# Performance work log

Measured on AMD Instinct MI355X. Metric: run time of the kernel, lower is better.

Reference implementation:

```python
import jax, jax.numpy as jnp
import numpy as np

B, N, D, H, S = 64, 1000, 512, 8, 20
DK = D // H
TANH_CLIP = 10.0
NEG = -1e9


def setup_inputs() -> dict:
    key = jax.random.key(0)
    k1, k2, k3, k4, k5 = jax.random.split(key, 5)
    embeddings = jax.random.normal(k1, (B, N, D), dtype=jnp.float32)
    q = jax.random.normal(k2, (B, S, D), dtype=jnp.float32)
    # action_mask: True = feasible. Ensure at least one feasible node per row.
    action_mask = jax.random.bernoulli(k3, 0.5, (B, S, N))
    action_mask = action_mask.at[:, :, 0].set(True)
    W_kvl = jax.random.normal(k4, (D, 3 * D), dtype=jnp.float32) * (1.0 / np.sqrt(D))
    W_out = jax.random.normal(k5, (D, D), dtype=jnp.float32) * (1.0 / np.sqrt(D))
    return {"embeddings": embeddings, "q": q, "action_mask": action_mask,
            "W_kvl": W_kvl, "W_out": W_out}


def reference(embeddings, q, action_mask, W_kvl, W_out):
    # _precompute: project node embeddings into glimpse K, V and logit K
    kvl = jnp.einsum('bnd,de->bne', embeddings, W_kvl)  # [B,N,3D]
    glimpse_k, glimpse_v, logit_k = jnp.split(kvl, 3, axis=-1)
    # dynamic embedding is zero (StaticEmbedding for TSP)

    mask = ~action_mask  # True = infeasible, shape [B,S,N]

    # multi-head glimpse attention
    qh = q.reshape(B, S, H, DK)
    kh = glimpse_k.reshape(B, N, H, DK)
    vh = glimpse_v.reshape(B, N, H, DK)
    compat = jnp.einsum('bshd,bnhd->bhsn', qh, kh) / np.sqrt(DK)
    compat = jnp.where(mask[:, None, :, :], NEG, compat)
    attn = jax.nn.softmax(compat, axis=-1)
    heads = jnp.einsum('bhsn,bnhd->bshd', attn, vh).reshape(B, S, D)
    glimpse = jnp.einsum('bsd,de->bse', heads, W_out)  # [B,S,D]

    # pointer logits against logit_k, tanh clipping, mask, log-softmax
    logits = jnp.einsum('bsd,bnd->bsn', glimpse, logit_k) / np.sqrt(D)
    logits = TANH_CLIP * jnp.tanh(logits)
    logits = jnp.where(mask, NEG, logits)
    log_p = jax.nn.log_softmax(logits, axis=-1)  # [B,S,N]

    # rearrange 'b s l -> (s b) l'
    return jnp.swapaxes(log_p, 0, 1).reshape(S * B, N)
```

## Files before the change

### kernel.cpp

```cpp
#include <hip/hip_runtime.h>

#define BB 64
#define NN 1000
#define NP 1024
#define DD 512
#define HH 8
#define SS 20
#define NEGV -1e9f

typedef float v4f __attribute__((ext_vector_type(4)));
typedef short v8s __attribute__((ext_vector_type(8)));
typedef int   v8i __attribute__((ext_vector_type(8)));
typedef int   v4i __attribute__((ext_vector_type(4)));
typedef unsigned char uchar;
typedef unsigned long long ulong_t;

static __device__ __forceinline__ short f2bf(float f) {
    unsigned u = __builtin_bit_cast(unsigned, f);
    u = (u + 0x7fffu + ((u >> 16) & 1u)) >> 16;
    return (short)u;
}
static __device__ __forceinline__ float bf2f(short s) {
    unsigned u = ((unsigned)(unsigned short)s) << 16;
    return __builtin_bit_cast(float, u);
}
static __device__ __forceinline__ uchar f2fp8(float f) {
    return (uchar)(__builtin_amdgcn_cvt_pk_fp8_f32(f, 0.f, 0, false) & 0xff);
}

static __device__ __forceinline__ void gld16(const void* g, void* l) {
    __builtin_amdgcn_global_load_lds(
        (const __attribute__((address_space(1))) void*)(g),
        (__attribute__((address_space(3))) void*)(l),
        16, 0, 0);
}

__global__ void prep(const float* __restrict__ Wkvl, uchar* __restrict__ Wt8,
                     const float* __restrict__ Wout, short* __restrict__ Wot,
                     const float* __restrict__ emb, int* __restrict__ emb8) {
    __shared__ float t[32][33];
    int bid = blockIdx.x, tid = threadIdx.x;
    if (bid < 768) {
        int c0 = (bid % 48) * 32, r0 = (bid / 48) * 32;
        int x = tid & 31, y = tid >> 5;
        for (int k = 0; k < 32; k += 8)
            t[y + k][x] = Wkvl[(long)(r0 + y + k) * 1536 + c0 + x];
        __syncthreads();
        for (int k = 0; k < 32; k += 8)
            Wt8[(long)(c0 + y + k) * 512 + r0 + x] = f2fp8(t[x][y + k]);
    } else if (bid < 1024) {
        int bb = bid - 768;
        int c0 = (bb & 15) * 32, r0 = (bb >> 4) * 32;
        int x = tid & 31, y = tid >> 5;
        for (int k = 0; k < 32; k += 8)
            t[y + k][x] = Wout[(long)(r0 + y + k) * 512 + c0 + x];
        __syncthreads();
        for (int k = 0; k < 32; k += 8)
            Wot[(long)(c0 + y + k) * 512 + r0 + x] = f2bf(t[x][y + k]);
    } else {
        int i = (bid - 1024) * 256 + tid;
        long o = (long)i * 8;
        v4f a = *(const v4f*)(emb + o);
        v4f b = *(const v4f*)(emb + o + 4);
        int lo = __builtin_amdgcn_cvt_pk_fp8_f32(a.x, a.y, 0, false);
        lo = __builtin_amdgcn_cvt_pk_fp8_f32(a.z, a.w, lo, true);
        int hi = __builtin_amdgcn_cvt_pk_fp8_f32(b.x, b.y, 0, false);
        hi = __builtin_amdgcn_cvt_pk_fp8_f32(b.z, b.w, hi, true);
        int2 r; r.x = lo; r.y = hi;
        *(int2*)(emb8 + i * 2) = r;
    }
}

__global__ __launch_bounds__(256) void gemm_kvl(const uchar* __restrict__ emb8,
                                                const uchar* __restrict__ Wt8,
                                                uchar* __restrict__ kvl8) {
    extern __shared__ __align__(16) uchar smem[];
    uchar* As0 = smem;
    uchar* Bs0 = smem + 32768;
    int tid = threadIdx.x;
    int id = blockIdx.x;
    int wgid = (id & 7) * 750 + (id >> 3);
    int m_idx = wgid / 12, n_idx = wgid - m_idx * 12;
    int m0 = m_idx * 128, n0 = n_idx * 128;
    int wid = tid >> 6, lane = tid & 63, quad = lane >> 4, l16 = lane & 15;
    int wm = wid & 1, wn = wid >> 1;
    const uchar* Ag = emb8 + (long)m0 * 512;
    const uchar* Bg = Wt8 + (long)n0 * 512;
    int rsub = lane >> 3;
    int kc = ((lane & 7) ^ rsub) * 16;

    v4f acc[4][4] = {};

    auto stageAB = [&](int bi, int kk) {
        #pragma unroll
        for (int p = 0; p < 4; ++p) {
            int rl = wid * 32 + p * 8;
            gld16(Ag + (long)(rl + rsub) * 512 + kk + kc, As0 + bi * 16384 + rl * 128);
        }
        #pragma unroll
        for (int p = 0; p < 4; ++p) {
            int rl = wid * 32 + p * 8;
            gld16(Bg + (long)(rl + rsub) * 512 + kk + kc, Bs0 + bi * 16384 + rl * 128);
        }
    };
    auto ldfrag = [&](const uchar* base, int row) -> v8i {
        int c0 = (quad * 2) ^ (row & 7);
        v4i lo = *(const v4i*)(base + row * 128 + c0 * 16);
        v4i hi = *(const v4i*)(base + row * 128 + (c0 ^ 1) * 16);
        return __builtin_shufflevector(lo, hi, 0, 1, 2, 3, 4, 5, 6, 7);
    };

    stageAB(0, 0);
    stageAB(1, 128);
    asm volatile("s_waitcnt vmcnt(8)" ::: "memory");
    __builtin_amdgcn_s_barrier();
    __builtin_amdgcn_sched_barrier(0);

    v8i af[4], bf[4];
    #pragma unroll
    for (int t = 0; t < 4; ++t) {
        int cur = t & 1;
        const uchar* ab = As0 + cur * 16384;
        const uchar* bb = Bs0 + cur * 16384;
        #pragma unroll
        for (int i = 0; i < 4; ++i) af[i] = ldfrag(ab, wm * 64 + i * 16 + l16);
        #pragma unroll
        for (int j = 0; j < 4; ++j) bf[j] = ldfrag(bb, wn * 64 + j * 16 + l16);
        __builtin_amdgcn_s_setprio(1);
        #pragma unroll
        for (int i = 0; i < 4; ++i)
            #pragma unroll
            for (int j = 0; j < 2; ++j)
                acc[i][j] = __builtin_amdgcn_mfma_scale_f32_16x16x128_f8f6f4(
                    af[i], bf[j], acc[i][j], 0, 0, 0, 0x7f7f7f7f, 0, 0x7f7f7f7f);
        __builtin_amdgcn_s_setprio(0);
        asm volatile("s_waitcnt lgkmcnt(0)" ::: "memory");
        __builtin_amdgcn_s_barrier();
        if (t < 2) stageAB(cur, (t + 2) * 128);
        __builtin_amdgcn_s_setprio(1);
        #pragma unroll
        for (int i = 0; i < 4; ++i)
            #pragma unroll
            for (int j = 2; j < 4; ++j)
                acc[i][j] = __builtin_amdgcn_mfma_scale_f32_16x16x128_f8f6f4(
                    af[i], bf[j], acc[i][j], 0, 0, 0, 0x7f7f7f7f, 0, 0x7f7f7f7f);
        __builtin_amdgcn_s_setprio(0);
        if (t < 3) {
            if (t < 2) asm volatile("s_waitcnt vmcnt(8)" ::: "memory");
            else       asm volatile("s_waitcnt vmcnt(0)" ::: "memory");
            __builtin_amdgcn_s_barrier();
            __builtin_amdgcn_sched_barrier(0);
        }
    }
    __syncthreads();

    short* rp = (short*)smem;
    short* r = rp + wid * (16 * 72);
    #pragma unroll
    for (int i = 0; i < 4; ++i) {
        #pragma unroll
        for (int jj = 0; jj < 4; ++jj)
            #pragma unroll
            for (int rr = 0; rr < 4; ++rr)
                r[(quad * 4 + rr) * 72 + jj * 16 + l16] = f2bf(acc[i][jj][rr]);
        #pragma unroll
        for (int h = 0; h < 2; ++h) {
            int rowl = h * 8 + (lane >> 3);
            int colc = (lane & 7) * 8;
            v8s val = *(const v8s*)(r + rowl * 72 + colc);
            int lo = __builtin_amdgcn_cvt_pk_fp8_f32(bf2f(val[0]), bf2f(val[1]), 0, false);
            lo = __builtin_amdgcn_cvt_pk_fp8_f32(bf2f(val[2]), bf2f(val[3]), lo, true);
            int hi = __builtin_amdgcn_cvt_pk_fp8_f32(bf2f(val[4]), bf2f(val[5]), 0, false);
            hi = __builtin_amdgcn_cvt_pk_fp8_f32(bf2f(val[6]), bf2f(val[7]), hi, true);
            int2 st; st.x = lo; st.y = hi;
            *(int2*)(kvl8 + (long)(m0 + wm * 64 + i * 16 + rowl) * 1536 +
                     n0 + wn * 64 + colc) = st;
        }
    }
}

__global__ void transpose_v(const uchar* __restrict__ kvl8, uchar* __restrict__ Vt8) {
    int bh = blockIdx.x, b = bh >> 3, h = bh & 7;
    int n0 = blockIdx.y * 64;
    __shared__ uchar T[64][72];
    int tid = threadIdx.x;
    #pragma unroll
    for (int it = 0; it < 2; ++it) {
        int nl = (tid >> 3) + it * 32;
        int n = n0 + nl;
        int nc = n < NN ? n : NN - 1;
        int d0 = (tid & 7) * 8;
        ulong_t v = *(const ulong_t*)(kvl8 + ((long)b * NN + nc) * 1536 + DD + h * 64 + d0);
        uchar* vb = (uchar*)&v;
        #pragma unroll
        for (int j = 0; j < 8; ++j) T[d0 + j][nl] = vb[j];
    }
    __syncthreads();
    #pragma unroll
    for (int it = 0; it < 2; ++it) {
        int d = (tid >> 3) + it * 32;
        int ns = (tid & 7) * 8;
        *(ulong_t*)(Vt8 + ((long)bh * 64 + d) * NP + n0 + ns) = *(const ulong_t*)&T[d][ns];
    }
}

#define CST 1036
__global__ __launch_bounds__(512) void attn_fused(const float* __restrict__ q,
                                                  const uchar* __restrict__ kvl8,
                                                  const uchar* __restrict__ Vt8,
                                                  const int* __restrict__ mask,
                                                  float* __restrict__ heads) {
    int b = blockIdx.x, h = blockIdx.y;
    __shared__ __align__(16) uchar qs[32 * 72];
    __shared__ __align__(16) short cmp[SS * CST];
    int tid = threadIdx.x, wid = tid >> 6, lane = tid & 63, quad = lane >> 4, l16 = lane & 15;
    for (int i = tid; i < 32 * 64; i += 512) {
        int row = i >> 6, col = i & 63;
        float v = (row < SS) ? q[((long)b * SS + row) * DD + h * 64 + col] : 0.f;
        qs[row * 72 + col] = f2fp8(v);
    }
    __syncthreads();
    long af[2][2];
    #pragma unroll
    for (int mt = 0; mt < 2; ++mt)
        #pragma unroll
        for (int ks = 0; ks < 2; ++ks)
            af[mt][ks] = *(const long*)(qs + (mt * 16 + l16) * 72 + ks * 32 + quad * 8);
    for (int t = 0; t < 8; ++t) {
        int nt = wid * 8 + t;
        int n = nt * 16 + l16;
        int nc = n < NN ? n : NN - 1;
        const uchar* kp = kvl8 + ((long)b * NN + nc) * 1536 + h * 64 + quad * 8;
        long b0 = *(const long*)kp;
        long b1 = *(const long*)(kp + 32);
        #pragma unroll
        for (int mt = 0; mt < 2; ++mt) {
            v4f a = {};
            a = __builtin_amdgcn_mfma_f32_16x16x32_fp8_fp8(af[mt][0], b0, a, 0, 0, 0);
            a = __builtin_amdgcn_mfma_f32_16x16x32_fp8_fp8(af[mt][1], b1, a, 0, 0, 0);
            #pragma unroll
            for (int r = 0; r < 4; ++r) {
                int s = mt * 16 + quad * 4 + r;
                if (s < SS) cmp[s * CST + nt * 16 + l16] = f2bf(a[r] * 0.125f);
            }
        }
    }
    __syncthreads();
    for (int s = wid; s < SS; s += 8) {
        const int* mr = mask + ((long)b * SS + s) * NN;
        float x[16];
        float mx = NEGV;
        #pragma unroll
        for (int i = 0; i < 16; ++i) {
            int n = lane + 64 * i;
            float v = bf2f(cmp[s * CST + n]);
            bool feas = (n < NN) && (mr[n < NN ? n : 0] != 0);
            x[i] = feas ? v : NEGV;
            mx = fmaxf(mx, x[i]);
        }
        for (int off = 32; off; off >>= 1) mx = fmaxf(mx, __shfl_xor(mx, off));
        float sum = 0.f;
        #pragma unroll
        for (int i = 0; i < 16; ++i) { x[i] = __expf(x[i] - mx); sum += x[i]; }
        for (int off = 32; off; off >>= 1) sum += __shfl_xor(sum, off);
        float inv = 1.0f / sum;
        uchar* pr = (uchar*)cmp + (long)s * (CST * 2);
        #pragma unroll
        for (int i = 0; i < 16; ++i) pr[lane + 64 * i] = f2fp8(x[i] * inv);
    }
    __syncthreads();
    int mt = wid & 1, dt = wid >> 1;
    int srow = mt * 16 + l16; if (srow > SS - 1) srow = SS - 1;
    const uchar* ap = (const uchar*)cmp + (long)srow * (CST * 2) + quad * 8;
    const uchar* vb = Vt8 + (long)(b * HH + h) * 64 * NP;
    v4f acc = {};
    for (int k0 = 0; k0 < NP; k0 += 32) {
        long afr = *(const long*)(ap + k0);
        long bfr = *(const long*)(vb + (long)(dt * 16 + l16) * NP + k0 + quad * 8);
        acc = __builtin_amdgcn_mfma_f32_16x16x32_fp8_fp8(afr, bfr, acc, 0, 0, 0);
    }
    #pragma unroll
    for (int r = 0; r < 4; ++r) {
        int s = mt * 16 + quad * 4 + r;
        if (s < SS)
            heads[((long)b * SS + s) * DD + h * 64 + dt * 16 + l16] = acc[r];
    }
}

__global__ __launch_bounds__(256) void out_proj(const float* __restrict__ heads,
                                                const short* __restrict__ Wot,
                                                float* __restrict__ glimpse) {
    __shared__ __align__(16) short As[64 * 40], Bs[64 * 40];
    int tid = threadIdx.x;
    int m0 = blockIdx.x * 64, n0 = blockIdx.y * 64;
    int wid = tid >> 6, lane = tid & 63, quad = lane >> 4, l16 = lane & 15;
    int wm = wid & 1, wn = wid >> 1;
    int arow = tid >> 3, akol = (tid & 7) * 4;
    int brow = tid >> 2, bkol = (tid & 3) * 8;
    v4f acc[2][2] = {};
    for (int kk = 0; kk < 512; kk += 32) {
        #pragma unroll
        for (int p = 0; p < 2; ++p) {
            int r = arow + p * 32;
            v4f a = *(const v4f*)(heads + (long)(m0 + r) * 512 + kk + akol);
            short4 s4;
            s4.x = f2bf(a.x); s4.y = f2bf(a.y); s4.z = f2bf(a.z); s4.w = f2bf(a.w);
            *(short4*)(As + r * 40 + akol) = s4;
        }
        *(uint4*)(Bs + brow * 40 + bkol) =
            *(const uint4*)(Wot + (long)(n0 + brow) * 512 + kk + bkol);
        __syncthreads();
        #pragma unroll
        for (int i = 0; i < 2; ++i) {
            v8s af = *(const v8s*)(As + (wm * 32 + i * 16 + l16) * 40 + quad * 8);
            #pragma unroll
            for (int j = 0; j < 2; ++j) {
                v8s bf = *(const v8s*)(Bs + (wn * 32 + j * 16 + l16) * 40 + quad * 8);
                acc[i][j] = __builtin_amdgcn_mfma_f32_16x16x32_bf16(af, bf, acc[i][j], 0, 0, 0);
            }
        }
        __syncthreads();
    }
    #pragma unroll
    for (int i = 0; i < 2; ++i)
        #pragma unroll
        for (int j = 0; j < 2; ++j)
            #pragma unroll
            for (int r = 0; r < 4; ++r)
                glimpse[(long)(m0 + wm * 32 + i * 16 + quad * 4 + r) * 512 +
                        n0 + wn * 32 + j * 16 + l16] = acc[i][j][r];
}

__global__ __launch_bounds__(256) void ptr_logits(const float* __restrict__ glimpse,
                                                  const uchar* __restrict__ kvl8,
                                                  float* __restrict__ logits) {
    int b = blockIdx.x, g = blockIdx.y;
    __shared__ __align__(16) uchar Gs[32 * 520];
    int tid = threadIdx.x;
    #pragma unroll
    for (int it = 0; it < 16; ++it) {
        int e = it * 1024 + tid * 4;
        int row = e >> 9, col = e & 511;
        int pk = 0;
        if (row < SS) {
            v4f a = *(const v4f*)(glimpse + ((long)b * SS + row) * 512 + col);
            pk = __builtin_amdgcn_cvt_pk_fp8_f32(a.x, a.y, 0, false);
            pk = __builtin_amdgcn_cvt_pk_fp8_f32(a.z, a.w, pk, true);
        }
        *(int*)(Gs + row * 520 + col) = pk;
    }
    __syncthreads();
    int wid = tid >> 6, lane = tid & 63, quad = lane >> 4, l16 = lane & 15;
    const float scale = 0.04419417382415922f;
    int nt = g * 4 + wid;
    int n = nt * 16 + l16;
    int ncl = n < NN ? n : NN - 1;
    const uchar* kp = kvl8 + ((long)b * NN + ncl) * 1536 + 1024 + quad * 8;
    v4f acc[2] = {};
    for (int k = 0; k < 16; ++k) {
        long bfr = *(const long*)(kp + k * 32);
        #pragma unroll
        for (int m = 0; m < 2; ++m) {
            long afr = *(const long*)(Gs + (m * 16 + l16) * 520 + k * 32 + quad * 8);
            acc[m] = __builtin_amdgcn_mfma_f32_16x16x32_fp8_fp8(afr, bfr, acc[m], 0, 0, 0);
        }
    }
    #pragma unroll
    for (int m = 0; m < 2; ++m)
        #pragma unroll
        for (int r = 0; r < 4; ++r) {
            int s = m * 16 + quad * 4 + r;
            if (s < SS)
                logits[((long)b * SS + s) * NP + nt * 16 + l16] = acc[m][r] * scale;
        }
}

__global__ __launch_bounds__(256) void logsoftmax_out(const float* __restrict__ logits,
                                                      const int* __restrict__ mask,
                                                      float* __restrict__ out) {
    int row = blockIdx.x;
    int b = row / SS, s = row % SS;
    int tid = threadIdx.x;
    __shared__ float red[8];
    int n0 = tid * 4;
    v4f v = *(const v4f*)(logits + (long)row * NP + n0);
    const int* mr = mask + (long)row * NN;
    float x[4];
    float mx = NEGV;
    #pragma unroll
    for (int j = 0; j < 4; ++j) {
        int n = n0 + j;
        float t = 10.f * tanhf(v[j]);
        bool feas = (n < NN) && (mr[n < NN ? n : 0] != 0);
        x[j] = feas ? t : NEGV;
        mx = fmaxf(mx, x[j]);
    }
    for (int off = 32; off; off >>= 1) mx = fmaxf(mx, __shfl_xor(mx, off));
    int wid = tid >> 6, lane = tid & 63;
    if (lane == 0) red[wid] = mx;
    __syncthreads();
    mx = fmaxf(fmaxf(red[0], red[1]), fmaxf(red[2], red[3]));
    float sum = 0.f;
    #pragma unroll
    for (int j = 0; j < 4; ++j) sum += __expf(x[j] - mx);
    for (int off = 32; off; off >>= 1) sum += __shfl_xor(sum, off);
    __syncthreads();
    if (lane == 0) red[4 + wid] = sum;
    __syncthreads();
    sum = red[4] + red[5] + red[6] + red[7];
    float lse = mx + __logf(sum);
    float* orow = out + ((long)s * BB + b) * NN;
    #pragma unroll
    for (int j = 0; j < 4; ++j) {
        int n = n0 + j;
        if (n < NN) orow[n] = x[j] - lse;
    }
}

extern "C" void kernel_launch(void* const* d_in, const int* in_sizes, int n_in,
                              void* d_out, int out_size, void* d_ws, size_t ws_size,
                              hipStream_t stream) {
    const float* emb  = (const float*)d_in[0];
    const float* q    = (const float*)d_in[1];
    const int*   mask = (const int*)d_in[2];
    const float* Wkvl = (const float*)d_in[3];
    const float* Wout = (const float*)d_in[4];
    float* out = (float*)d_out;

    char* ws = (char*)d_ws;
    uchar* kvl8    = (uchar*)ws; ws += (size_t)64000 * 1536;
    uchar* Vt8     = (uchar*)ws; ws += (size_t)512 * 64 * NP;
    uchar* Wt8     = (uchar*)ws; ws += (size_t)1536 * 512;
    uchar* emb8    = (uchar*)ws; ws += (size_t)64000 * 512;
    short* Wot     = (short*)ws; ws += (size_t)512 * 512 * 2;
    float* heads   = (float*)ws; ws += (size_t)BB * SS * DD * 4;
    float* glimpse = (float*)ws; ws += (size_t)BB * SS * DD * 4;
    float* logits  = (float*)ws; ws += (size_t)BB * SS * NP * 4;

    static int s_attr_done = 0;
    if (!s_attr_done) {
        hipFuncSetAttribute(reinterpret_cast<const void*>(gemm_kvl),
                            hipFuncAttributeMaxDynamicSharedMemorySize, 65536);
        s_attr_done = 1;
    }

    prep<<<dim3(1024 + 16000), 256, 0, stream>>>(Wkvl, Wt8, Wout, Wot, emb, (int*)emb8);
    gemm_kvl<<<dim3(6000), 256, 65536, stream>>>(emb8, Wt8, kvl8);
    transpose_v<<<dim3(512, 16), 256, 0, stream>>>(kvl8, Vt8);
    attn_fused<<<dim3(BB, HH), 512, 0, stream>>>(q, kvl8, Vt8, mask, heads);
    out_proj<<<dim3(20, 8), 256, 0, stream>>>(heads, Wot, glimpse);
    ptr_logits<<<dim3(BB, 16), 256, 0, stream>>>(glimpse, kvl8, logits);
    logsoftmax_out<<<dim3(BB * SS), 256, 0, stream>>>(logits, mask, out);
}
```

Before: 349.2 us.

## Pre-pack K and V into MFMA fragment layout for coalesced attention loads

Replaces the V-only transpose kernel with a pack kernel that writes both glimpse K and transposed V in a per-lane MFMA fragment order. The attention kernel then reads each fragment as one contiguous 512-byte wave load, instead of strided 8-byte reads across 1536-byte rows. The packed K buffer reuses the Wt8 and emb8 workspace, which is free once the projection GEMM has finished. The cost is an extra K write and read pass in the pack kernel.

```diff
diff --git a/kernel.cpp b/kernel.cpp
--- a/kernel.cpp
+++ b/kernel.cpp
@@ -179,35 +179,46 @@
     }
 }
 
-__global__ void transpose_v(const uchar* __restrict__ kvl8, uchar* __restrict__ Vt8) {
+__global__ void pack_kv(const uchar* __restrict__ kvl8, uchar* __restrict__ Kf,
+                        uchar* __restrict__ Vf) {
     int bh = blockIdx.x, b = bh >> 3, h = bh & 7;
-    int n0 = blockIdx.y * 64;
-    __shared__ uchar T[64][72];
+    int g = blockIdx.y;
+    __shared__ uchar Kl[64][72];
+    __shared__ uchar VT[64][72];
     int tid = threadIdx.x;
-    #pragma unroll
-    for (int it = 0; it < 2; ++it) {
-        int nl = (tid >> 3) + it * 32;
-        int n = n0 + nl;
-        int nc = n < NN ? n : NN - 1;
-        int d0 = (tid & 7) * 8;
-        ulong_t v = *(const ulong_t*)(kvl8 + ((long)b * NN + nc) * 1536 + DD + h * 64 + d0);
-        uchar* vb = (uchar*)&v;
-        #pragma unroll
-        for (int j = 0; j < 8; ++j) T[d0 + j][nl] = vb[j];
-    }
-    __syncthreads();
-    #pragma unroll
-    for (int it = 0; it < 2; ++it) {
-        int d = (tid >> 3) + it * 32;
-        int ns = (tid & 7) * 8;
-        *(ulong_t*)(Vt8 + ((long)bh * 64 + d) * NP + n0 + ns) = *(const ulong_t*)&T[d][ns];
+    int node_l = tid >> 2, chunk = (tid & 3) * 16;
+    int gn = g * 64 + node_l;
+    int ncl = gn < NN ? gn : NN - 1;
+    const uchar* rowp = kvl8 + ((long)b * NN + ncl) * 1536 + h * 64;
+    *(v4i*)&Kl[node_l][chunk] = *(const v4i*)(rowp + chunk);
+    {
+        const uchar* vp = rowp + 512 + chunk;
+        ulong_t v0 = *(const ulong_t*)(vp);
+        ulong_t v1 = *(const ulong_t*)(vp + 8);
+        uchar* b0p = (uchar*)&v0; uchar* b1p = (uchar*)&v1;
+        #pragma unroll
+        for (int j = 0; j < 8; ++j) VT[chunk + j][node_l] = b0p[j];
+        #pragma unroll
+        for (int j = 0; j < 8; ++j) VT[chunk + 8 + j][node_l] = b1p[j];
+    }
+    __syncthreads();
+    int wid = tid >> 6, lane = tid & 63, l16 = lane & 15, quad = lane >> 4;
+    #pragma unroll
+    for (int ks = 0; ks < 2; ++ks) {
+        ulong_t frag = *(const ulong_t*)&Kl[wid * 16 + l16][ks * 32 + quad * 8];
+        *(ulong_t*)(Kf + (((long)bh * 64 + g * 4 + wid) * 2 + ks) * 512 + lane * 8) = frag;
+    }
+    #pragma unroll
+    for (int sub = 0; sub < 2; ++sub) {
+        ulong_t frag = *(const ulong_t*)&VT[wid * 16 + l16][sub * 32 + quad * 8];
+        *(ulong_t*)(Vf + (((long)bh * 4 + wid) * 32 + g * 2 + sub) * 512 + lane * 8) = frag;
     }
 }
 
 #define CST 1036
 __global__ __launch_bounds__(512) void attn_fused(const float* __restrict__ q,
-                                                  const uchar* __restrict__ kvl8,
-                                                  const uchar* __restrict__ Vt8,
+                                                  const uchar* __restrict__ Kf,
+                                                  const uchar* __restrict__ Vf,
                                                   const int* __restrict__ mask,
                                                   float* __restrict__ heads) {
     int b = blockIdx.x, h = blockIdx.y;
@@ -226,13 +237,11 @@
         #pragma unroll
         for (int ks = 0; ks < 2; ++ks)
             af[mt][ks] = *(const long*)(qs + (mt * 16 + l16) * 72 + ks * 32 + quad * 8);
+    const uchar* kfb = Kf + ((long)(b * HH + h) * 64) * 1024;
     for (int t = 0; t < 8; ++t) {
         int nt = wid * 8 + t;
-        int n = nt * 16 + l16;
-        int nc = n < NN ? n : NN - 1;
-        const uchar* kp = kvl8 + ((long)b * NN + nc) * 1536 + h * 64 + quad * 8;
-        long b0 = *(const long*)kp;
-        long b1 = *(const long*)(kp + 32);
+        long b0 = *(const long*)(kfb + (long)nt * 1024 + lane * 8);
+        long b1 = *(const long*)(kfb + (long)nt * 1024 + 512 + lane * 8);
         #pragma unroll
         for (int mt = 0; mt < 2; ++mt) {
             v4f a = {};
@@ -272,11 +281,11 @@
     int mt = wid & 1, dt = wid >> 1;
     int srow = mt * 16 + l16; if (srow > SS - 1) srow = SS - 1;
     const uchar* ap = (const uchar*)cmp + (long)srow * (CST * 2) + quad * 8;
-    const uchar* vb = Vt8 + (long)(b * HH + h) * 64 * NP;
+    const uchar* vfb = Vf + (((long)(b * HH + h) * 4 + dt) * 32) * 512;
     v4f acc = {};
-    for (int k0 = 0; k0 < NP; k0 += 32) {
-        long afr = *(const long*)(ap + k0);
-        long bfr = *(const long*)(vb + (long)(dt * 16 + l16) * NP + k0 + quad * 8);
+    for (int k0s = 0; k0s < 32; ++k0s) {
+        long afr = *(const long*)(ap + k0s * 32);
+        long bfr = *(const long*)(vfb + (long)k0s * 512 + lane * 8);
         acc = __builtin_amdgcn_mfma_f32_16x16x32_fp8_fp8(afr, bfr, acc, 0, 0, 0);
     }
     #pragma unroll
@@ -437,6 +446,9 @@
     float* glimpse = (float*)ws; ws += (size_t)BB * SS * DD * 4;
     float* logits  = (float*)ws; ws += (size_t)BB * SS * NP * 4;
 
+    uchar* Kf = Wt8;
+    uchar* Vf = Vt8;
+
     static int s_attr_done = 0;
     if (!s_attr_done) {
         hipFuncSetAttribute(reinterpret_cast<const void*>(gemm_kvl),
@@ -446,8 +458,8 @@
 
     prep<<<dim3(1024 + 16000), 256, 0, stream>>>(Wkvl, Wt8, Wout, Wot, emb, (int*)emb8);
     gemm_kvl<<<dim3(6000), 256, 65536, stream>>>(emb8, Wt8, kvl8);
-    transpose_v<<<dim3(512, 16), 256, 0, stream>>>(kvl8, Vt8);
-    attn_fused<<<dim3(BB, HH), 512, 0, stream>>>(q, kvl8, Vt8, mask, heads);
+    pack_kv<<<dim3(512, 16), 256, 0, stream>>>(kvl8, Kf, Vf);
+    attn_fused<<<dim3(BB, HH), 512, 0, stream>>>(q, Kf, Vf, mask, heads);
     out_proj<<<dim3(20, 8), 256, 0, stream>>>(heads, Wot, glimpse);
     ptr_logits<<<dim3(BB, 16), 256, 0, stream>>>(glimpse, kvl8, logits);
     logsoftmax_out<<<dim3(BB * SS), 256, 0, stream>>>(logits, mask, out);
```

After: 349.2 us. No clear change (+0.0%).
